# Performance work log

Measured on AMD Instinct MI355X. Metric: run time of the kernel, lower is better.

Reference implementation:

```python
import jax, jax.numpy as jnp
import numpy as np

N_LAT, N_LON = 121, 240
N = N_LAT * N_LON          # 29040 nodes (fixed by module's reshape)
DEG = 16
E = N * DEG                # 464640 edges
H = 128                    # input_nf = output_nf = hidden_nf
LV = 11                    # pressure levels (coord_mlp outputs 11*2)
EDGE_IN = 2 * H + 34       # source + target + w_diff(33) + edge_attr(1)


def setup_inputs() -> dict:
    key = jax.random.key(0)
    ks = jax.random.split(key, 18)
    def w(k, shape, s=0.05):
        return jax.random.normal(k, shape, dtype=jnp.float32) * s
    return {
        'h': w(ks[0], (N, H), 1.0),
        'u': w(ks[1], (N, LV), 1.0),
        'v': w(ks[2], (N, LV), 1.0),
        'edge_attr': w(ks[3], (E, 1), 1.0),
        # edge MLP: Linear(EDGE_IN,H) ReLU Linear(H,H) ReLU
        'W_e1': w(ks[4], (EDGE_IN, H)), 'b_e1': jnp.zeros((H,), jnp.float32),
        'W_e2': w(ks[5], (H, H)),       'b_e2': jnp.zeros((H,), jnp.float32),
        # node MLP: Linear(2H+H,H) ReLU Linear(H,H)
        'W_n1': w(ks[6], (3 * H, H)),   'b_n1': jnp.zeros((H,), jnp.float32),
        'W_n2': w(ks[7], (H, H)),       'b_n2': jnp.zeros((H,), jnp.float32),
        # coord MLP: Linear(H,H) ReLU Linear(H,22,bias=False) with tiny xavier gain
        'W_c1': w(ks[8], (H, H)),       'b_c1': jnp.zeros((H,), jnp.float32),
        'W_cl': w(ks[9], (H, 2 * LV), 0.001),
        'edge_index': jax.random.randint(ks[10], (2, E), 0, N, dtype=jnp.int32),
    }


def reference(h, u, v, edge_attr,
              W_e1, b_e1, W_e2, b_e2,
              W_n1, b_n1, W_n2, b_n2,
              W_c1, b_c1, W_cl,
              edge_index):
    row, col = edge_index[0], edge_index[1]

    # ---- coord2radial ----
    uc, vc = u[col], v[col]          # [E, LV]
    ur, vr = u[row], v[row]
    col_speed = jnp.sqrt(uc * uc + vc * vc)
    row_speed = jnp.sqrt(ur * ur + vr * vr)
    rel_dirt = (uc * ur + vc * vr) / (col_speed * row_speed)
    w_diff = jnp.concatenate([rel_dirt, col_speed, row_speed], axis=1)  # [E, 33]

    # ---- edge model ----
    edge_in = jnp.concatenate([h[row], h[col], w_diff, edge_attr], axis=1)  # [E, EDGE_IN]
    edge_feat = jax.nn.relu(jax.nn.relu(edge_in @ W_e1 + b_e1) @ W_e2 + b_e2)  # [E, H]

    # ---- node model (scatter-sum + lat-band mean pooling) ----
    agg = jax.ops.segment_sum(edge_feat, row, num_segments=N)  # [N, H]
    lat = agg.reshape(N_LAT, N_LON, H).mean(axis=1, keepdims=True)  # [121,1,H]
    lat_agg = jnp.broadcast_to(lat, (N_LAT, N_LON, H)).reshape(N, H)
    node_in = jnp.concatenate([h, agg, lat_agg], axis=1)  # [N, 3H]
    h_out = jax.nn.relu(node_in @ W_n1 + b_n1) @ W_n2 + b_n2 + h  # residual

    # ---- coord model (scatter-mean with clamp) ----
    ef = (jax.nn.relu(edge_feat @ W_c1 + b_c1) @ W_cl).reshape(E, 2, LV)
    radial = jnp.stack([uc, vc], axis=1)                 # [E, 2, LV]
    rad2 = jnp.sqrt(jnp.sum(radial * radial, axis=-1))   # [E, 2] (per-component magnitude)
    wind = ef * rad2[:, :, None]                         # [E, 2, LV]
    cnt = jnp.maximum(
        jax.ops.segment_sum(jnp.ones((E,), jnp.float32), row, num_segments=N), 1.0)[:, None]
    agg_u = jnp.clip(jax.ops.segment_sum(wind[:, 0, :], row, num_segments=N) / cnt, -100.0, 100.0)
    agg_v = jnp.clip(jax.ops.segment_sum(wind[:, 1, :], row, num_segments=N) / cnt, -100.0, 100.0)

    return h_out, agg_u, agg_v
```

## Files before the change

### kernel.cpp

```cpp
#include <hip/hip_runtime.h>
#include <hip/hip_bf16.h>
#include <math.h>

#define NN   29040
#define NLAT 121
#define NLON 240
#define HD   128
#define LVN  11
#define EE   464640

typedef __attribute__((ext_vector_type(8))) short short8;
typedef __attribute__((ext_vector_type(16))) float f16v;

#define OFF_WE1 0
#define OFF_WE2 40960
#define OFF_WC1 57344
#define OFF_WCL 73728
#define OFF_WN1 77824
#define OFF_WN2 126976
#define WP_SHORTS 143360

__device__ inline short f2b(float x) {
    union { __hip_bfloat16 b; short s; } v;
    v.b = __float2bfloat16(x);
    return v.s;
}
__device__ inline float b2f(unsigned short b) {
    union { unsigned u; float f; } v; v.u = ((unsigned)b) << 16;
    return v.f;
}

#define SB_HIST  1815
#define SB_HCAST 1815
#define SB_UV    114
#define SB_WP    70

__global__ __launch_bounds__(256)
void setup_kernel(const int* __restrict__ eidx, int* __restrict__ cnt,
                  const float* __restrict__ h, short* __restrict__ hb,
                  const float* __restrict__ u, const float* __restrict__ v,
                  float* __restrict__ uvrec,
                  const float* __restrict__ We1, const float* __restrict__ We2,
                  const float* __restrict__ Wc1, const float* __restrict__ Wcl,
                  const float* __restrict__ Wn1, const float* __restrict__ Wn2,
                  short* __restrict__ wp)
{
    const int b = blockIdx.x, tid = threadIdx.x;
    if (b < SB_HIST) {
        int e = b * 256 + tid;
        atomicAdd(&cnt[eidx[e]], 1);
        return;
    }
    if (b < SB_HIST + SB_HCAST) {
        int idx = (b - SB_HIST) * 256 + tid;
        const float4* hf = (const float4*)h;
        float4 a = hf[idx * 2], c = hf[idx * 2 + 1];
        short8 o;
        o[0] = f2b(a.x); o[1] = f2b(a.y); o[2] = f2b(a.z); o[3] = f2b(a.w);
        o[4] = f2b(c.x); o[5] = f2b(c.y); o[6] = f2b(c.z); o[7] = f2b(c.w);
        ((short8*)hb)[idx] = o;
        return;
    }
    if (b < SB_HIST + SB_HCAST + SB_UV) {
        int n = (b - SB_HIST - SB_HCAST) * 256 + tid;
        if (n >= NN) return;
        float* r = uvrec + (size_t)n * 36;
        float un = 0.f, vn = 0.f;
#pragma unroll
        for (int l = 0; l < LVN; ++l) {
            float uu = u[n * LVN + l], vv = v[n * LVN + l];
            float s = sqrtf(uu * uu + vv * vv);
            r[l]      = uu / s;
            r[11 + l] = vv / s;
            r[22 + l] = s;
            un += uu * uu; vn += vv * vv;
        }
        r[33] = sqrtf(un);
        r[34] = sqrtf(vn);
        r[35] = 0.f;
        return;
    }
    {
        int fg = (b - SB_HIST - SB_HCAST - SB_UV) * 4 + (tid >> 6);
        const int l = tid & 63;
        int kind, f, base;
        if (fg < 80)       { kind = 0; f = fg;       base = OFF_WE1; }
        else if (fg < 112) { kind = 1; f = fg - 80;  base = OFF_WE2; }
        else if (fg < 144) { kind = 2; f = fg - 112; base = OFF_WC1; }
        else if (fg < 152) { kind = 3; f = fg - 144; base = OFF_WCL; }
        else if (fg < 248) { kind = 4; f = fg - 152; base = OFF_WN1; }
        else               { kind = 5; f = fg - 248; base = OFF_WN2; }
        const int nfw = (kind == 3) ? 1 : 4;
        const int kf = f / nfw, nf = f % nfw;
        short* dst = wp + base + (size_t)f * 512 + l * 8;
        for (int i = 0; i < 8; ++i) {
            int k = kf * 16 + ((l >> 5) << 3) + i;
            int n = nf * 32 + (l & 31);
            float val = 0.f;
            if (kind == 0) {
                int r = (k < 33) ? (256 + k) : (k == 33 ? 289 : (k < 64 ? -1 : k - 64));
                if (r >= 0) val = We1[r * HD + n];
            } else if (kind == 1) val = We2[k * HD + n];
            else if (kind == 2)  val = Wc1[k * HD + n];
            else if (kind == 3)  { if (n < 22) val = Wcl[k * 22 + n]; }
            else if (kind == 4)  val = Wn1[k * HD + n];
            else                 val = Wn2[k * HD + n];
            dst[i] = f2b(val);
        }
    }
}

__global__ __launch_bounds__(1024)
void scan_kernel(const int* __restrict__ cnt, int* __restrict__ off)
{
    __shared__ int part[1024];
    const int tid = threadIdx.x;
    const int CH = 29;
    int lo = tid * CH, hi = min(lo + CH, NN);
    int s = 0;
    for (int i = lo; i < hi; ++i) s += cnt[i];
    part[tid] = s;
    __syncthreads();
    for (int d = 1; d < 1024; d <<= 1) {
        int vv = (tid >= d) ? part[tid - d] : 0;
        __syncthreads();
        part[tid] += vv;
        __syncthreads();
    }
    int run = (tid == 0) ? 0 : part[tid - 1];
    for (int i = lo; i < hi; ++i) { off[i] = run; run += cnt[i]; }
    if (tid == 1023) off[NN] = run;
}

__global__ __launch_bounds__(256)
void scatter_kernel(const int* __restrict__ eidx, const int* __restrict__ off,
                    int* __restrict__ cur, int* __restrict__ csr)
{
    int e = blockIdx.x * 256 + threadIdx.x;
    if (e >= EE) return;
    int row = eidx[e];
    int p = atomicAdd(&cur[row], 1);
    csr[off[row] + p] = e;
}

template<int KF, int NFL, int NJ>
__device__ inline void gemm32_lds(const short* At, const short* Wp, int nf0,
                                  const float* bias, f16v* acc,
                                  int mrow, int colbase, int r31, int kh, int lane)
{
    const char* arow = (const char*)At + mrow * 256;
    const int sw = (mrow & 7) << 4;
#pragma unroll
    for (int j = 0; j < NJ; ++j) {
        float bv = bias ? bias[colbase + j * 32 + r31] : 0.f;
#pragma unroll
        for (int q = 0; q < 16; ++q) acc[j][q] = bv;
    }
#pragma unroll
    for (int kf = 0; kf < KF; ++kf) {
        short8 a = *(const short8*)(arow + ((kf * 32 + 16 * kh) ^ sw));
#pragma unroll
        for (int j = 0; j < NJ; ++j) {
            short8 bfr = *(const short8*)(Wp + (size_t)(kf * NFL + nf0 + j) * 512 + lane * 8);
            acc[j] = __builtin_amdgcn_mfma_f32_32x32x16_bf16(a, bfr, acc[j], 0, 0, 0);
        }
    }
}

template<int NJ>
__device__ inline void store32(short* tile, const f16v* acc, int rg, int colbase,
                               int r31, int kh, bool relu)
{
#pragma unroll
    for (int j = 0; j < NJ; ++j)
#pragma unroll
        for (int reg = 0; reg < 16; ++reg) {
            int row = rg * 32 + (reg & 3) + 8 * (reg >> 2) + 4 * kh;
            int cb2 = (colbase + j * 32 + r31) * 2;
            float vv = acc[j][reg];
            if (relu) vv = fmaxf(vv, 0.f);
            *(short*)((char*)tile + row * 256 + (cb2 ^ ((row & 7) << 4))) = f2b(vv);
        }
}

__global__ __launch_bounds__(256, 4)
void edge_mfma(const short* __restrict__ hb, const float* __restrict__ uvrec,
               const float* __restrict__ ea,
               const float* __restrict__ be1, const float* __restrict__ be2,
               const float* __restrict__ bc1,
               const short* __restrict__ wp,
               const int* __restrict__ eidx, const int* __restrict__ csr,
               float* __restrict__ agg, float* __restrict__ aggu,
               float* __restrict__ aggv)
{
    __shared__ short Twd[64 * 64];
    __shared__ short T1[64 * 128];
    __shared__ int   rows_s[64];
    __shared__ float radu_s[64], radv_s[64];

    const int tid = threadIdx.x, lane = tid & 63, w = tid >> 6;
    const int rg = w >> 1, cg = w & 1;
    const int e0 = blockIdx.x * 64;
    const int r31 = lane & 31, kh = lane >> 5;
    const int mrow = rg * 32 + r31;
    const int sw = (mrow & 7) << 4;
    const int colbase = cg * 64;

    int e1 = csr[e0 + mrow];
    int rowm = eidx[e1], colm = eidx[EE + e1];
    const short* hr = hb + (size_t)rowm * HD + 8 * kh;
    const short* hc = hb + (size_t)colm * HD + 8 * kh;

    {
        const int m2 = tid >> 2, q = tid & 3;
        const int sw2 = (m2 & 7) << 4;
        int e2 = csr[e0 + m2];
        int row2 = eidx[e2], col2 = eidx[EE + e2];
        const float* rc = uvrec + (size_t)col2 * 36;
        const float* rr = uvrec + (size_t)row2 * 36;
        char* arow = (char*)(Twd + m2 * 64);
        short8 z = {0, 0, 0, 0, 0, 0, 0, 0};
        *(short8*)(arow + q * 32) = z;
        *(short8*)(arow + q * 32 + 16) = z;
        for (int l = q; l < LVN; l += 4) {
            float rel = rc[l] * rr[l] + rc[11 + l] * rr[11 + l];
            *(short*)(arow + ((2 * l) ^ sw2))        = f2b(rel);
            *(short*)(arow + ((2 * (11 + l)) ^ sw2)) = f2b(rc[22 + l]);
            *(short*)(arow + ((2 * (22 + l)) ^ sw2)) = f2b(rr[22 + l]);
        }
        if (q == 0) { rows_s[m2] = row2; radu_s[m2] = rc[33]; radv_s[m2] = rc[34]; }
        if (q == 3) *(short*)(arow + ((2 * 33) ^ sw2)) = f2b(ea[e2]);
    }
    __syncthreads();

    f16v acc[2];
#pragma unroll
    for (int j = 0; j < 2; ++j) {
        float bv = be1[colbase + j * 32 + r31];
#pragma unroll
        for (int q = 0; q < 16; ++q) acc[j][q] = bv;
    }
    {
        const char* awd = (const char*)(Twd + mrow * 64);
#pragma unroll
        for (int kf = 0; kf < 4; ++kf) {
            short8 a = *(const short8*)(awd + ((kf * 32 + 16 * kh) ^ sw));
#pragma unroll
            for (int j = 0; j < 2; ++j) {
                short8 bfr = *(const short8*)(wp + OFF_WE1 + (size_t)(kf * 4 + cg * 2 + j) * 512 + lane * 8);
                acc[j] = __builtin_amdgcn_mfma_f32_32x32x16_bf16(a, bfr, acc[j], 0, 0, 0);
            }
        }
#pragma unroll
        for (int s = 0; s < 8; ++s) {
            short8 a = *(const short8*)(hr + s * 16);
#pragma unroll
            for (int j = 0; j < 2; ++j) {
                short8 bfr = *(const short8*)(wp + OFF_WE1 + (size_t)((s + 4) * 4 + cg * 2 + j) * 512 + lane * 8);
                acc[j] = __builtin_amdgcn_mfma_f32_32x32x16_bf16(a, bfr, acc[j], 0, 0, 0);
            }
        }
#pragma unroll
        for (int s = 0; s < 8; ++s) {
            short8 a = *(const short8*)(hc + s * 16);
#pragma unroll
            for (int j = 0; j < 2; ++j) {
                short8 bfr = *(const short8*)(wp + OFF_WE1 + (size_t)((s + 12) * 4 + cg * 2 + j) * 512 + lane * 8);
                acc[j] = __builtin_amdgcn_mfma_f32_32x32x16_bf16(a, bfr, acc[j], 0, 0, 0);
            }
        }
    }
    store32<2>(T1, acc, rg, colbase, r31, kh, true);
    __syncthreads();

    gemm32_lds<8, 4, 2>(T1, wp + OFF_WE2, cg * 2, be2, acc, mrow, colbase, r31, kh, lane);
    __syncthreads();
    store32<2>(T1, acc, rg, colbase, r31, kh, true);
    __syncthreads();

    gemm32_lds<8, 4, 2>(T1, wp + OFF_WC1, cg * 2, bc1, acc, mrow, colbase, r31, kh, lane);

    {
        const int col = colbase + lane;
        const int m0 = rg * 32;
        int curr = rows_s[m0];
        float s = 0.f;
        for (int m = m0; m < m0 + 32; ++m) {
            int r = rows_s[m];
            float vv = b2f(*(const unsigned short*)((const char*)T1 + m * 256 + (((col & 127) * 2) ^ ((m & 7) << 4))));
            if (r != curr) { atomicAdd(&agg[(size_t)curr * HD + (col & 127)], s); s = 0.f; curr = r; }
            s += vv;
        }
        atomicAdd(&agg[(size_t)curr * HD + (col & 127)], s);
    }
    __syncthreads();
    store32<2>(T1, acc, rg, colbase, r31, kh, true);
    __syncthreads();

    if (cg == 0) {
        gemm32_lds<8, 1, 1>(T1, wp + OFF_WCL, 0, (const float*)nullptr, acc, mrow, 0, r31, kh, lane);
        float* O22 = (float*)Twd;
#pragma unroll
        for (int reg = 0; reg < 16; ++reg) {
            int row = rg * 32 + (reg & 3) + 8 * (reg >> 2) + 4 * kh;
            O22[row * 32 + r31] = acc[0][reg];
        }
        const int c = r31;
        if (c < 22) {
            const bool isU = c < LVN;
            const int lvl = isU ? c : c - LVN;
            float* dst = isU ? aggu : aggv;
            const float* radp = isU ? radu_s : radv_s;
            const int m0 = rg * 32 + kh * 16;
            int curr = rows_s[m0]; float s = 0.f;
            for (int m = m0; m < m0 + 16; ++m) {
                int r = rows_s[m];
                float vv = O22[m * 32 + c] * radp[m];
                if (r != curr) { atomicAdd(&dst[(size_t)curr * LVN + lvl], s); s = 0.f; curr = r; }
                s += vv;
            }
            atomicAdd(&dst[(size_t)curr * LVN + lvl], s);
        }
    }
}

__global__ __launch_bounds__(256)
void post_kernel(const float* __restrict__ agg, short* __restrict__ latb,
                 float* __restrict__ aggu, float* __restrict__ aggv,
                 const int* __restrict__ off)
{
    const int b = blockIdx.x, tid = threadIdx.x;
    if (b < NLAT) {
        __shared__ float part[256];
        const int j = tid & 127, half = tid >> 7;
        float s = 0.f;
        for (int lon = half * 120; lon < (half + 1) * 120; ++lon)
            s += agg[((size_t)b * NLON + lon) * HD + j];
        part[tid] = s;
        __syncthreads();
        if (tid < 128)
            latb[(size_t)b * HD + tid] = f2b((part[tid] + part[128 + tid]) * (1.0f / NLON));
        return;
    }
    int tt = (b - NLAT) * 256 + tid;
    if (tt >= NN * LVN) return;
    int n = tt / LVN;
    float c = fmaxf((float)(off[n + 1] - off[n]), 1.f);
    float xu = aggu[tt] / c, xv = aggv[tt] / c;
    aggu[tt] = fminf(fmaxf(xu, -100.f), 100.f);
    aggv[tt] = fminf(fmaxf(xv, -100.f), 100.f);
}

__global__ __launch_bounds__(512, 4)
void node_mfma(const short* __restrict__ hb, const float* __restrict__ h,
               const short* __restrict__ latb,
               const float* __restrict__ bn1, const float* __restrict__ bn2,
               const short* __restrict__ wp, float* __restrict__ out)
{
    __shared__ short T1[128 * 128];
    const int tid = threadIdx.x, lane = tid & 63, w = tid >> 6;
    const int rg = w >> 1, cg = w & 1;
    const int r31 = lane & 31, kh = lane >> 5;
    const int mrow = rg * 32 + r31;
    const int colbase = cg * 64;
    const int n0 = blockIdx.x * 128;
    const int n = n0 + mrow;
    const int nc = (n < NN) ? n : (NN - 1);
    const short* hp = hb + (size_t)nc * HD + 8 * kh;
    const float* ap = out + (size_t)nc * HD + 8 * kh;
    const short* lp = latb + (size_t)(nc / NLON) * HD + 8 * kh;

    f16v acc[2];
#pragma unroll
    for (int j = 0; j < 2; ++j) {
        float bv = bn1[colbase + j * 32 + r31];
#pragma unroll
        for (int q = 0; q < 16; ++q) acc[j][q] = bv;
    }
#pragma unroll
    for (int s = 0; s < 8; ++s) {
        short8 a = *(const short8*)(hp + s * 16);
#pragma unroll
        for (int j = 0; j < 2; ++j) {
            short8 bfr = *(const short8*)(wp + OFF_WN1 + (size_t)(s * 4 + cg * 2 + j) * 512 + lane * 8);
            acc[j] = __builtin_amdgcn_mfma_f32_32x32x16_bf16(a, bfr, acc[j], 0, 0, 0);
        }
    }
#pragma unroll
    for (int s = 0; s < 8; ++s) {
        short8 a;
#pragma unroll
        for (int q = 0; q < 8; ++q) a[q] = f2b(ap[s * 16 + q]);
#pragma unroll
        for (int j = 0; j < 2; ++j) {
            short8 bfr = *(const short8*)(wp + OFF_WN1 + (size_t)((s + 8) * 4 + cg * 2 + j) * 512 + lane * 8);
            acc[j] = __builtin_amdgcn_mfma_f32_32x32x16_bf16(a, bfr, acc[j], 0, 0, 0);
        }
    }
#pragma unroll
    for (int s = 0; s < 8; ++s) {
        short8 a = *(const short8*)(lp + s * 16);
#pragma unroll
        for (int j = 0; j < 2; ++j) {
            short8 bfr = *(const short8*)(wp + OFF_WN1 + (size_t)((s + 16) * 4 + cg * 2 + j) * 512 + lane * 8);
            acc[j] = __builtin_amdgcn_mfma_f32_32x32x16_bf16(a, bfr, acc[j], 0, 0, 0);
        }
    }
    store32<2>(T1, acc, rg, colbase, r31, kh, true);
    __syncthreads();
    gemm32_lds<8, 4, 2>(T1, wp + OFF_WN2, cg * 2, bn2, acc, mrow, colbase, r31, kh, lane);

#pragma unroll
    for (int j = 0; j < 2; ++j)
#pragma unroll
        for (int reg = 0; reg < 16; ++reg) {
            int row = rg * 32 + (reg & 3) + 8 * (reg >> 2) + 4 * kh;
            int gn = n0 + row;
            if (gn < NN) {
                int col = colbase + j * 32 + r31;
                out[(size_t)gn * HD + col] = acc[j][reg] + h[(size_t)gn * HD + col];
            }
        }
}

extern "C" void kernel_launch(void* const* d_in, const int* in_sizes, int n_in,
                              void* d_out, int out_size, void* d_ws, size_t ws_size,
                              hipStream_t stream)
{
    const float* h   = (const float*)d_in[0];
    const float* u   = (const float*)d_in[1];
    const float* v   = (const float*)d_in[2];
    const float* ea  = (const float*)d_in[3];
    const float* We1 = (const float*)d_in[4];
    const float* be1 = (const float*)d_in[5];
    const float* We2 = (const float*)d_in[6];
    const float* be2 = (const float*)d_in[7];
    const float* Wn1 = (const float*)d_in[8];
    const float* bn1 = (const float*)d_in[9];
    const float* Wn2 = (const float*)d_in[10];
    const float* bn2 = (const float*)d_in[11];
    const float* Wc1 = (const float*)d_in[12];
    const float* bc1 = (const float*)d_in[13];
    const float* Wcl = (const float*)d_in[14];
    const int*   eidx = (const int*)d_in[15];

    float* out  = (float*)d_out;
    float* agg  = out;
    float* aggu = out + (size_t)NN * HD;
    float* aggv = aggu + (size_t)NN * LVN;

    char* p = (char*)d_ws;
    short* wp  = (short*)p;                  p += (size_t)WP_SHORTS * 2;
    int*   off = (int*)p;                    p += (size_t)(NN + 1) * 4;
    int*   csr = (int*)p;                    p += (size_t)EE * 4;
    p = (char*)(((size_t)p + 15) & ~(size_t)15);
    short* hb  = (short*)p;                  p += (size_t)NN * HD * 2;
    float* uvr = (float*)p;                  p += (size_t)NN * 36 * 4;
    short* latb = (short*)p;                 p += (size_t)NLAT * HD * 2;
    p = (char*)(((size_t)p + 15) & ~(size_t)15);
    int*   cnt = (int*)p;                    p += (size_t)NN * 4;
    int*   cur = (int*)p;

    hipMemsetAsync(d_out, 0, (size_t)out_size * sizeof(float), stream);
    hipMemsetAsync(cnt, 0, (size_t)2 * NN * sizeof(int), stream);

    setup_kernel<<<SB_HIST + SB_HCAST + SB_UV + SB_WP, 256, 0, stream>>>(
        eidx, cnt, h, hb, u, v, uvr, We1, We2, Wc1, Wcl, Wn1, Wn2, wp);
    scan_kernel<<<1, 1024, 0, stream>>>(cnt, off);
    scatter_kernel<<<EE / 256, 256, 0, stream>>>(eidx, off, cur, csr);

    edge_mfma<<<EE / 64, 256, 0, stream>>>(hb, uvr, ea, be1, be2, bc1,
                                           wp, eidx, csr, agg, aggu, aggv);

    post_kernel<<<NLAT + (NN * LVN + 255) / 256, 256, 0, stream>>>(
        agg, latb, aggu, aggv, off);

    node_mfma<<<(NN + 127) / 128, 512, 0, stream>>>(hb, h, latb, bn1, bn2, wp, agg);
}
```

Before: 294.6 us.

## Process 128 edges per block so each weight fragment feeds two MFMAs

```diff
diff --git a/kernel.cpp b/kernel.cpp
--- a/kernel.cpp
+++ b/kernel.cpp
@@ -143,47 +143,55 @@
     csr[off[row] + p] = e;
 }
 
-template<int KF, int NFL, int NJ>
-__device__ inline void gemm32_lds(const short* At, const short* Wp, int nf0,
-                                  const float* bias, f16v* acc,
-                                  int mrow, int colbase, int r31, int kh, int lane)
-{
-    const char* arow = (const char*)At + mrow * 256;
-    const int sw = (mrow & 7) << 4;
-#pragma unroll
-    for (int j = 0; j < NJ; ++j) {
-        float bv = bias ? bias[colbase + j * 32 + r31] : 0.f;
-#pragma unroll
-        for (int q = 0; q < 16; ++q) acc[j][q] = bv;
-    }
-#pragma unroll
-    for (int kf = 0; kf < KF; ++kf) {
-        short8 a = *(const short8*)(arow + ((kf * 32 + 16 * kh) ^ sw));
+
+template<int NFL, int NJ>
+__device__ inline void gemm_t1(const short* T1, const short* Wp, int nf0,
+                               const float* bias, f16v* acc,
+                               int row0, int colbase, int r31, int kh, int lane)
+{
+    const int sw = (row0 & 7) << 4;
+    const char* a0p = (const char*)T1 + row0 * 256;
+    const char* a1p = a0p + 32 * 256;
+#pragma unroll
+    for (int m = 0; m < 2; ++m)
 #pragma unroll
         for (int j = 0; j < NJ; ++j) {
-            short8 bfr = *(const short8*)(Wp + (size_t)(kf * NFL + nf0 + j) * 512 + lane * 8);
-            acc[j] = __builtin_amdgcn_mfma_f32_32x32x16_bf16(a, bfr, acc[j], 0, 0, 0);
+            float bv = bias ? bias[colbase + j * 32 + r31] : 0.f;
+#pragma unroll
+            for (int q = 0; q < 16; ++q) acc[m * NJ + j][q] = bv;
+        }
+#pragma unroll
+    for (int kf = 0; kf < 8; ++kf) {
+        short8 a0 = *(const short8*)(a0p + ((kf * 32 + 16 * kh) ^ sw));
+        short8 a1 = *(const short8*)(a1p + ((kf * 32 + 16 * kh) ^ sw));
+#pragma unroll
+        for (int j = 0; j < NJ; ++j) {
+            short8 b = *(const short8*)(Wp + (size_t)(kf * NFL + nf0 + j) * 512 + lane * 8);
+            acc[0 * NJ + j] = __builtin_amdgcn_mfma_f32_32x32x16_bf16(a0, b, acc[0 * NJ + j], 0, 0, 0);
+            acc[1 * NJ + j] = __builtin_amdgcn_mfma_f32_32x32x16_bf16(a1, b, acc[1 * NJ + j], 0, 0, 0);
         }
     }
 }
 
 template<int NJ>
-__device__ inline void store32(short* tile, const f16v* acc, int rg, int colbase,
-                               int r31, int kh, bool relu)
-{
-#pragma unroll
-    for (int j = 0; j < NJ; ++j)
-#pragma unroll
-        for (int reg = 0; reg < 16; ++reg) {
-            int row = rg * 32 + (reg & 3) + 8 * (reg >> 2) + 4 * kh;
-            int cb2 = (colbase + j * 32 + r31) * 2;
-            float vv = acc[j][reg];
-            if (relu) vv = fmaxf(vv, 0.f);
-            *(short*)((char*)tile + row * 256 + (cb2 ^ ((row & 7) << 4))) = f2b(vv);
-        }
-}
-
-__global__ __launch_bounds__(256, 4)
+__device__ inline void store_mj(short* tile, const f16v* acc, int rwbase, int colbase,
+                                int r31, int kh, bool relu)
+{
+#pragma unroll
+    for (int m = 0; m < 2; ++m)
+#pragma unroll
+        for (int j = 0; j < NJ; ++j)
+#pragma unroll
+            for (int reg = 0; reg < 16; ++reg) {
+                int row = rwbase + 32 * m + (reg & 3) + 8 * (reg >> 2) + 4 * kh;
+                int cb2 = (colbase + j * 32 + r31) * 2;
+                float vv = acc[m * NJ + j][reg];
+                if (relu) vv = fmaxf(vv, 0.f);
+                *(short*)((char*)tile + row * 256 + (cb2 ^ ((row & 7) << 4))) = f2b(vv);
+            }
+}
+
+__global__ __launch_bounds__(256, 3)
 void edge_mfma(const short* __restrict__ hb, const float* __restrict__ uvrec,
                const float* __restrict__ ea,
                const float* __restrict__ be1, const float* __restrict__ be2,
@@ -193,26 +201,29 @@
                float* __restrict__ agg, float* __restrict__ aggu,
                float* __restrict__ aggv)
 {
-    __shared__ short Twd[64 * 64];
-    __shared__ short T1[64 * 128];
-    __shared__ int   rows_s[64];
-    __shared__ float radu_s[64], radv_s[64];
+    __shared__ short Twd[128 * 64];
+    __shared__ short T1[128 * 128];
+    __shared__ int   rows_s[128];
+    __shared__ float radu_s[128], radv_s[128];
 
     const int tid = threadIdx.x, lane = tid & 63, w = tid >> 6;
-    const int rg = w >> 1, cg = w & 1;
-    const int e0 = blockIdx.x * 64;
+    const int rw = w >> 1, cg = w & 1;
+    const int e0 = blockIdx.x * 128;
     const int r31 = lane & 31, kh = lane >> 5;
-    const int mrow = rg * 32 + r31;
-    const int sw = (mrow & 7) << 4;
+    const int row0 = rw * 64 + r31;
+    const int sw = (row0 & 7) << 4;
     const int colbase = cg * 64;
 
-    int e1 = csr[e0 + mrow];
-    int rowm = eidx[e1], colm = eidx[EE + e1];
-    const short* hr = hb + (size_t)rowm * HD + 8 * kh;
-    const short* hc = hb + (size_t)colm * HD + 8 * kh;
-
-    {
-        const int m2 = tid >> 2, q = tid & 3;
+    int ea1 = csr[e0 + row0], eb1 = csr[e0 + row0 + 32];
+    int rowa = eidx[ea1], cola = eidx[EE + ea1];
+    int rowb = eidx[eb1], colb = eidx[EE + eb1];
+    const short* hr0 = hb + (size_t)rowa * HD + 8 * kh;
+    const short* hc0 = hb + (size_t)cola * HD + 8 * kh;
+    const short* hr1 = hb + (size_t)rowb * HD + 8 * kh;
+    const short* hc1 = hb + (size_t)colb * HD + 8 * kh;
+
+    {
+        const int m2 = tid >> 1, q = tid & 1;
         const int sw2 = (m2 & 7) << 4;
         int e2 = csr[e0 + m2];
         int row2 = eidx[e2], col2 = eidx[EE + e2];
@@ -220,98 +231,120 @@
         const float* rr = uvrec + (size_t)row2 * 36;
         char* arow = (char*)(Twd + m2 * 64);
         short8 z = {0, 0, 0, 0, 0, 0, 0, 0};
-        *(short8*)(arow + q * 32) = z;
-        *(short8*)(arow + q * 32 + 16) = z;
-        for (int l = q; l < LVN; l += 4) {
+        *(short8*)(arow + q * 64) = z;
+        *(short8*)(arow + q * 64 + 16) = z;
+        *(short8*)(arow + q * 64 + 32) = z;
+        *(short8*)(arow + q * 64 + 48) = z;
+        for (int l = q; l < LVN; l += 2) {
             float rel = rc[l] * rr[l] + rc[11 + l] * rr[11 + l];
             *(short*)(arow + ((2 * l) ^ sw2))        = f2b(rel);
             *(short*)(arow + ((2 * (11 + l)) ^ sw2)) = f2b(rc[22 + l]);
             *(short*)(arow + ((2 * (22 + l)) ^ sw2)) = f2b(rr[22 + l]);
         }
-        if (q == 0) { rows_s[m2] = row2; radu_s[m2] = rc[33]; radv_s[m2] = rc[34]; }
-        if (q == 3) *(short*)(arow + ((2 * 33) ^ sw2)) = f2b(ea[e2]);
-    }
-    __syncthreads();
-
-    f16v acc[2];
-#pragma unroll
-    for (int j = 0; j < 2; ++j) {
-        float bv = be1[colbase + j * 32 + r31];
-#pragma unroll
-        for (int q = 0; q < 16; ++q) acc[j][q] = bv;
-    }
-    {
-        const char* awd = (const char*)(Twd + mrow * 64);
+        if (q == 0) {
+            rows_s[m2] = row2; radu_s[m2] = rc[33]; radv_s[m2] = rc[34];
+            *(short*)(arow + ((2 * 33) ^ sw2)) = f2b(ea[e2]);
+        }
+    }
+    __syncthreads();
+
+    f16v acc[4];
+#pragma unroll
+    for (int m = 0; m < 2; ++m)
+#pragma unroll
+        for (int j = 0; j < 2; ++j) {
+            float bv = be1[colbase + j * 32 + r31];
+#pragma unroll
+            for (int q = 0; q < 16; ++q) acc[m * 2 + j][q] = bv;
+        }
+    {
+        const char* awd0 = (const char*)Twd + row0 * 128;
+        const char* awd1 = awd0 + 32 * 128;
 #pragma unroll
         for (int kf = 0; kf < 4; ++kf) {
-            short8 a = *(const short8*)(awd + ((kf * 32 + 16 * kh) ^ sw));
+            short8 a0 = *(const short8*)(awd0 + ((kf * 32 + 16 * kh) ^ sw));
+            short8 a1 = *(const short8*)(awd1 + ((kf * 32 + 16 * kh) ^ sw));
 #pragma unroll
             for (int j = 0; j < 2; ++j) {
-                short8 bfr = *(const short8*)(wp + OFF_WE1 + (size_t)(kf * 4 + cg * 2 + j) * 512 + lane * 8);
-                acc[j] = __builtin_amdgcn_mfma_f32_32x32x16_bf16(a, bfr, acc[j], 0, 0, 0);
+                short8 b = *(const short8*)(wp + OFF_WE1 + (size_t)(kf * 4 + cg * 2 + j) * 512 + lane * 8);
+                acc[j]     = __builtin_amdgcn_mfma_f32_32x32x16_bf16(a0, b, acc[j], 0, 0, 0);
+                acc[2 + j] = __builtin_amdgcn_mfma_f32_32x32x16_bf16(a1, b, acc[2 + j], 0, 0, 0);
             }
         }
 #pragma unroll
         for (int s = 0; s < 8; ++s) {
-            short8 a = *(const short8*)(hr + s * 16);
+            short8 a0 = *(const short8*)(hr0 + s * 16);
+            short8 a1 = *(const short8*)(hr1 + s * 16);
 #pragma unroll
             for (int j = 0; j < 2; ++j) {
-                short8 bfr = *(const short8*)(wp + OFF_WE1 + (size_t)((s + 4) * 4 + cg * 2 + j) * 512 + lane * 8);
-                acc[j] = __builtin_amdgcn_mfma_f32_32x32x16_bf16(a, bfr, acc[j], 0, 0, 0);
+                short8 b = *(const short8*)(wp + OFF_WE1 + (size_t)((s + 4) * 4 + cg * 2 + j) * 512 + lane * 8);
+                acc[j]     = __builtin_amdgcn_mfma_f32_32x32x16_bf16(a0, b, acc[j], 0, 0, 0);
+                acc[2 + j] = __builtin_amdgcn_mfma_f32_32x32x16_bf16(a1, b, acc[2 + j], 0, 0, 0);
             }
         }
 #pragma unroll
         for (int s = 0; s < 8; ++s) {
-            short8 a = *(const short8*)(hc + s * 16);
+            short8 a0 = *(const short8*)(hc0 + s * 16);
+            short8 a1 = *(const short8*)(hc1 + s * 16);
 #pragma unroll
             for (int j = 0; j < 2; ++j) {
-                short8 bfr = *(const short8*)(wp + OFF_WE1 + (size_t)((s + 12) * 4 + cg * 2 + j) * 512 + lane * 8);
-                acc[j] = __builtin_amdgcn_mfma_f32_32x32x16_bf16(a, bfr, acc[j], 0, 0, 0);
-            }
-        }
-    }
-    store32<2>(T1, acc, rg, colbase, r31, kh, true);
-    __syncthreads();
-
-    gemm32_lds<8, 4, 2>(T1, wp + OFF_WE2, cg * 2, be2, acc, mrow, colbase, r31, kh, lane);
-    __syncthreads();
-    store32<2>(T1, acc, rg, colbase, r31, kh, true);
-    __syncthreads();
-
-    gemm32_lds<8, 4, 2>(T1, wp + OFF_WC1, cg * 2, bc1, acc, mrow, colbase, r31, kh, lane);
-
-    {
-        const int col = colbase + lane;
-        const int m0 = rg * 32;
-        int curr = rows_s[m0];
-        float s = 0.f;
-        for (int m = m0; m < m0 + 32; ++m) {
-            int r = rows_s[m];
-            float vv = b2f(*(const unsigned short*)((const char*)T1 + m * 256 + (((col & 127) * 2) ^ ((m & 7) << 4))));
-            if (r != curr) { atomicAdd(&agg[(size_t)curr * HD + (col & 127)], s); s = 0.f; curr = r; }
-            s += vv;
-        }
-        atomicAdd(&agg[(size_t)curr * HD + (col & 127)], s);
-    }
-    __syncthreads();
-    store32<2>(T1, acc, rg, colbase, r31, kh, true);
+                short8 b = *(const short8*)(wp + OFF_WE1 + (size_t)((s + 12) * 4 + cg * 2 + j) * 512 + lane * 8);
+                acc[j]     = __builtin_amdgcn_mfma_f32_32x32x16_bf16(a0, b, acc[j], 0, 0, 0);
+                acc[2 + j] = __builtin_amdgcn_mfma_f32_32x32x16_bf16(a1, b, acc[2 + j], 0, 0, 0);
+            }
+        }
+    }
+    store_mj<2>(T1, acc, rw * 64, colbase, r31, kh, true);
+    __syncthreads();
+
+    gemm_t1<4, 2>(T1, wp + OFF_WE2, cg * 2, be2, acc, row0, colbase, r31, kh, lane);
+    __syncthreads();
+    store_mj<2>(T1, acc, rw * 64, colbase, r31, kh, true);
+    __syncthreads();
+
+    gemm_t1<4, 2>(T1, wp + OFF_WC1, cg * 2, bc1, acc, row0, colbase, r31, kh, lane);
+
+    {
+        const int col = tid & 127;
+        for (int cc = (tid >> 7); cc < 4; cc += 2) {
+            const int m0 = cc * 32;
+            int curr = rows_s[m0]; float s = 0.f;
+            for (int m = m0; m < m0 + 32; ++m) {
+                int r = rows_s[m];
+                float vv = b2f(*(const unsigned short*)((const char*)T1 + m * 256 + ((col * 2) ^ ((m & 7) << 4))));
+                if (r != curr) { atomicAdd(&agg[(size_t)curr * HD + col], s); s = 0.f; curr = r; }
+                s += vv;
+            }
+            atomicAdd(&agg[(size_t)curr * HD + col], s);
+        }
+    }
+    __syncthreads();
+    store_mj<2>(T1, acc, rw * 64, colbase, r31, kh, true);
     __syncthreads();
 
     if (cg == 0) {
-        gemm32_lds<8, 1, 1>(T1, wp + OFF_WCL, 0, (const float*)nullptr, acc, mrow, 0, r31, kh, lane);
+        f16v acc2[2];
+        gemm_t1<1, 1>(T1, wp + OFF_WCL, 0, (const float*)nullptr, acc2, row0, 0, r31, kh, lane);
         float* O22 = (float*)Twd;
 #pragma unroll
-        for (int reg = 0; reg < 16; ++reg) {
-            int row = rg * 32 + (reg & 3) + 8 * (reg >> 2) + 4 * kh;
-            O22[row * 32 + r31] = acc[0][reg];
-        }
-        const int c = r31;
+        for (int m = 0; m < 2; ++m)
+#pragma unroll
+            for (int reg = 0; reg < 16; ++reg) {
+                int row = rw * 64 + 32 * m + (reg & 3) + 8 * (reg >> 2) + 4 * kh;
+                O22[row * 32 + r31] = acc2[m][reg];
+            }
+    }
+    __syncthreads();
+
+    {
+        const int c = tid & 31, ch = tid >> 5;
         if (c < 22) {
             const bool isU = c < LVN;
             const int lvl = isU ? c : c - LVN;
             float* dst = isU ? aggu : aggv;
             const float* radp = isU ? radu_s : radv_s;
-            const int m0 = rg * 32 + kh * 16;
+            const float* O22 = (const float*)Twd;
+            const int m0 = ch * 16;
             int curr = rows_s[m0]; float s = 0.f;
             for (int m = m0; m < m0 + 16; ++m) {
                 int r = rows_s[m];
@@ -362,6 +395,7 @@
     const int rg = w >> 1, cg = w & 1;
     const int r31 = lane & 31, kh = lane >> 5;
     const int mrow = rg * 32 + r31;
+    const int sw = (mrow & 7) << 4;
     const int colbase = cg * 64;
     const int n0 = blockIdx.x * 128;
     const int n = n0 + mrow;
@@ -406,10 +440,35 @@
             acc[j] = __builtin_amdgcn_mfma_f32_32x32x16_bf16(a, bfr, acc[j], 0, 0, 0);
         }
     }
-    store32<2>(T1, acc, rg, colbase, r31, kh, true);
-    __syncthreads();
-    gemm32_lds<8, 4, 2>(T1, wp + OFF_WN2, cg * 2, bn2, acc, mrow, colbase, r31, kh, lane);
-
+    {
+#pragma unroll
+        for (int j = 0; j < 2; ++j)
+#pragma unroll
+            for (int reg = 0; reg < 16; ++reg) {
+                int row = rg * 32 + (reg & 3) + 8 * (reg >> 2) + 4 * kh;
+                int cb2 = (colbase + j * 32 + r31) * 2;
+                *(short*)((char*)T1 + row * 256 + (cb2 ^ ((row & 7) << 4))) = f2b(fmaxf(acc[j][reg], 0.f));
+            }
+    }
+    __syncthreads();
+    {
+        const char* arow = (const char*)T1 + mrow * 256;
+#pragma unroll
+        for (int j = 0; j < 2; ++j) {
+            float bv = bn2[colbase + j * 32 + r31];
+#pragma unroll
+            for (int q = 0; q < 16; ++q) acc[j][q] = bv;
+        }
+#pragma unroll
+        for (int kf = 0; kf < 8; ++kf) {
+            short8 a = *(const short8*)(arow + ((kf * 32 + 16 * kh) ^ sw));
+#pragma unroll
+            for (int j = 0; j < 2; ++j) {
+                short8 bfr = *(const short8*)(wp + OFF_WN2 + (size_t)(kf * 4 + cg * 2 + j) * 512 + lane * 8);
+                acc[j] = __builtin_amdgcn_mfma_f32_32x32x16_bf16(a, bfr, acc[j], 0, 0, 0);
+            }
+        }
+    }
 #pragma unroll
     for (int j = 0; j < 2; ++j)
 #pragma unroll
@@ -469,8 +528,8 @@
     scan_kernel<<<1, 1024, 0, stream>>>(cnt, off);
     scatter_kernel<<<EE / 256, 256, 0, stream>>>(eidx, off, cur, csr);
 
-    edge_mfma<<<EE / 64, 256, 0, stream>>>(hb, uvr, ea, be1, be2, bc1,
-                                           wp, eidx, csr, agg, aggu, aggv);
+    edge_mfma<<<EE / 128, 256, 0, stream>>>(hb, uvr, ea, be1, be2, bc1,
+                                            wp, eidx, csr, agg, aggu, aggv);
 
     post_kernel<<<NLAT + (NN * LVN + 255) / 256, 256, 0, stream>>>(
         agg, latb, aggu, aggv, off);
```

After: 309.5 us. 5.1% more time.
